# Kernel tuning notes

Hardware: AMD Instinct MI355X
Metric: run time of the kernel (lower is better)

The kernel has to match this reference:

```python
import jax, jax.numpy as jnp
import numpy as np

B, S, D = 2, 2048, 1024
H, HD = 16, 64
DFF = 4 * D
EPS = 1e-5


def gelu(x):
    return 0.5 * x * (1.0 + jnp.tanh(jnp.sqrt(2.0 / jnp.pi) * (x + 0.044715 * x * x * x)))


def layer_norm(x, scale, bias):
    mu = jnp.mean(x, axis=-1, keepdims=True)
    var = jnp.mean(jnp.square(x - mu), axis=-1, keepdims=True)
    return (x - mu) * jax.lax.rsqrt(var + EPS) * scale + bias


def setup_inputs() -> dict:
    key = jax.random.key(0)
    ks = jax.random.split(key, 8)
    s = 0.02
    x = jax.random.normal(ks[0], (B, S, D), jnp.float32)
    mask = jnp.tril(jnp.ones((S, S), dtype=bool))[None, None]  # (1,1,S,S) causal
    return {
        "x": x,
        "mask": mask,
        "ln1_scale": jnp.ones((D,), jnp.float32),
        "ln1_bias": jnp.zeros((D,), jnp.float32),
        "ln2_scale": jnp.ones((D,), jnp.float32),
        "ln2_bias": jnp.zeros((D,), jnp.float32),
        "w_qkv": jax.random.normal(ks[1], (D, 3 * D), jnp.float32) * s,
        "b_qkv": jnp.zeros((3 * D,), jnp.float32),
        "w_attn_proj": jax.random.normal(ks[2], (D, D), jnp.float32) * s,
        "b_attn_proj": jnp.zeros((D,), jnp.float32),
        "w_fc": jax.random.normal(ks[3], (D, DFF), jnp.float32) * s,
        "b_fc": jnp.zeros((DFF,), jnp.float32),
        "w_mlp_proj": jax.random.normal(ks[4], (DFF, D), jnp.float32) * s,
        "b_mlp_proj": jnp.zeros((D,), jnp.float32),
    }


def reference(x, mask, ln1_scale, ln1_bias, ln2_scale, ln2_bias,
              w_qkv, b_qkv, w_attn_proj, b_attn_proj,
              w_fc, b_fc, w_mlp_proj, b_mlp_proj):
    bsz, seq, _ = x.shape
    # --- attention branch ---
    h = layer_norm(x, ln1_scale, ln1_bias)
    qkv = h @ w_qkv + b_qkv                       # (b, s, 3D)
    q, k, v = jnp.split(qkv, 3, axis=-1)
    q = q.reshape(bsz, seq, H, HD).transpose(0, 2, 1, 3)  # bhsd
    k = k.reshape(bsz, seq, H, HD).transpose(0, 2, 1, 3)
    v = v.reshape(bsz, seq, H, HD).transpose(0, 2, 1, 3)
    q = q * (1.0 / jnp.sqrt(HD))
    scores = jnp.einsum('bhqd,bhkd->bhqk', q, k)
    scores = jnp.where(mask, scores, -1e10)
    probs = jax.nn.softmax(scores, axis=-1)
    attn = jnp.einsum('bhqk,bhkd->bhqd', probs, v)
    attn = attn.transpose(0, 2, 1, 3).reshape(bsz, seq, D)
    attn = attn @ w_attn_proj + b_attn_proj
    x = x + attn
    # --- MLP branch ---
    h = layer_norm(x, ln2_scale, ln2_bias)
    h = gelu(h @ w_fc + b_fc)
    h = h @ w_mlp_proj + b_mlp_proj
    return x + h
```

## Files before the change

### kernel.cpp

```cpp
#include <hip/hip_runtime.h>
#include <stdint.h>


typedef __attribute__((ext_vector_type(8))) short bf16x8;
typedef __attribute__((ext_vector_type(8))) unsigned short u16x8;
typedef __attribute__((ext_vector_type(4))) float f32x4;

#define NEG_BIG -30000.0f
#define EXP2SC 0.18033688011112042f

__device__ __forceinline__ float b2f(unsigned short u) {
  union { unsigned int i; float f; } c; c.i = ((unsigned int)u) << 16; return c.f;
}
__device__ __forceinline__ unsigned short f2b(float f) {
  union { float f; unsigned int u; } c; c.f = f;
  unsigned int r = c.u + 0x7fffu + ((c.u >> 16) & 1u);
  return (unsigned short)(r >> 16);
}
__device__ __forceinline__ float ldx(const void* p, size_t i, int f32) {
  return f32 ? ((const float*)p)[i] : b2f(((const unsigned short*)p)[i]);
}
__device__ __forceinline__ void gld_lds16(const void* g, void* l) {
  __builtin_amdgcn_global_load_lds(
      (__attribute__((address_space(1))) void*)(void*)g,
      (__attribute__((address_space(3))) void*)l, 16, 0, 0);
}

__global__ void detect_k(const unsigned short* __restrict__ x, int* __restrict__ flag) {
  int lane = threadIdx.x;
  int cnt = 0;
#pragma unroll
  for (int j = 0; j < 4; ++j) {
    unsigned e = (x[lane * 4 + j] >> 7) & 0xFF;
    if (e >= 100 && e <= 145) cnt++;
  }
#pragma unroll
  for (int off = 32; off; off >>= 1) cnt += __shfl_down(cnt, off);
  if (lane == 0) *flag = (cnt < 220) ? 1 : 0;
}

__global__ __launch_bounds__(256) void transpose_k(
    const void* __restrict__ in, unsigned short* __restrict__ out,
    int K, int N, const int* __restrict__ flag) {
  int fm = *flag;
  __shared__ unsigned short tile[64][72];
  int n0 = blockIdx.x * 64, k0 = blockIdx.y * 64;
  int t = threadIdx.x;
  int r = t >> 3, c0 = (t & 7) * 8;
  if (fm) {
    const float* inf = (const float*)in;
#pragma unroll
    for (int p = 0; p < 2; ++p) {
      int k = r + p * 32;
      float4 v0 = *(const float4*)(inf + (size_t)(k0 + k) * N + n0 + c0);
      float4 v1 = *(const float4*)(inf + (size_t)(k0 + k) * N + n0 + c0 + 4);
      tile[k][c0 + 0] = f2b(v0.x); tile[k][c0 + 1] = f2b(v0.y);
      tile[k][c0 + 2] = f2b(v0.z); tile[k][c0 + 3] = f2b(v0.w);
      tile[k][c0 + 4] = f2b(v1.x); tile[k][c0 + 5] = f2b(v1.y);
      tile[k][c0 + 6] = f2b(v1.z); tile[k][c0 + 7] = f2b(v1.w);
    }
  } else {
    const unsigned short* inu = (const unsigned short*)in;
#pragma unroll
    for (int p = 0; p < 2; ++p) {
      int k = r + p * 32;
      u16x8 v = *(const u16x8*)(inu + (size_t)(k0 + k) * N + n0 + c0);
      *(u16x8*)&tile[k][c0] = v;
    }
  }
  __syncthreads();
#pragma unroll
  for (int p = 0; p < 2; ++p) {
    int n = r + p * 32;
    u16x8 v;
#pragma unroll
    for (int j = 0; j < 8; ++j) v[j] = tile[c0 + j][n];
    *(u16x8*)(out + (size_t)(n0 + n) * K + k0 + c0) = v;
  }
}

__global__ __launch_bounds__(256) void ln_k(
    const void* __restrict__ x, const void* __restrict__ sc,
    const void* __restrict__ bs, unsigned short* __restrict__ out,
    const int* __restrict__ flag, int xAdap) {
  int fm = *flag;
  int fx = xAdap ? fm : 0;
  int row = blockIdx.x, t = threadIdx.x;
  float f0, f1, f2, f3;
  if (fx) {
    float4 xv = ((const float4*)x)[(size_t)row * 256 + t];
    f0 = xv.x; f1 = xv.y; f2 = xv.z; f3 = xv.w;
  } else {
    ushort4 xv = ((const ushort4*)x)[(size_t)row * 256 + t];
    f0 = b2f(xv.x); f1 = b2f(xv.y); f2 = b2f(xv.z); f3 = b2f(xv.w);
  }
  float s = f0 + f1 + f2 + f3;
  float q = f0 * f0 + f1 * f1 + f2 * f2 + f3 * f3;
#pragma unroll
  for (int off = 32; off; off >>= 1) {
    s += __shfl_down(s, off);
    q += __shfl_down(q, off);
  }
  __shared__ float red[8];
  int w = t >> 6, lane = t & 63;
  if (lane == 0) { red[w] = s; red[w + 4] = q; }
  __syncthreads();
  float S = red[0] + red[1] + red[2] + red[3];
  float Q = red[4] + red[5] + red[6] + red[7];
  float mean = S * (1.f / 1024.f);
  float var = Q * (1.f / 1024.f) - mean * mean;
  float rstd = rsqrtf(var + 1e-5f);
  int c = t * 4;
  ushort4 o;
  o.x = f2b((f0 - mean) * rstd * ldx(sc, c, fm)     + ldx(bs, c, fm));
  o.y = f2b((f1 - mean) * rstd * ldx(sc, c + 1, fm) + ldx(bs, c + 1, fm));
  o.z = f2b((f2 - mean) * rstd * ldx(sc, c + 2, fm) + ldx(bs, c + 2, fm));
  o.w = f2b((f3 - mean) * rstd * ldx(sc, c + 3, fm) + ldx(bs, c + 3, fm));
  ((ushort4*)(out + (size_t)row * 1024))[t] = o;
}

template <int EPI>
__global__ __launch_bounds__(256) void gemm_bt(
    const unsigned short* __restrict__ A, const unsigned short* __restrict__ Bt,
    const void* __restrict__ bias, const void* __restrict__ res,
    void* __restrict__ C, int M, int N, int K,
    const int* __restrict__ flag, int resAdap, int outAdap) {
  int fm = *flag;
  int fr = resAdap ? fm : 0;
  int fo = outAdap ? fm : 0;
  __shared__ unsigned short As[128 * 32];
  __shared__ unsigned short Bs[128 * 32];
  int t = threadIdx.x;
  int bn = blockIdx.x * 128, bm = blockIdx.y * 128;
  int w = t >> 6, lane = t & 63, quad = lane >> 4, l16 = lane & 15;
  int wm = (w >> 1) * 64, wn = (w & 1) * 64;
  f32x4 acc[4][4] = {};

  int c1 = t, c2 = t + 256;
  int r1 = c1 >> 2, e1 = (c1 & 3) * 8;
  int r2 = c2 >> 2, e2 = (c2 & 3) * 8;
  const unsigned short* a1 = A + (size_t)(bm + r1) * K + e1;
  const unsigned short* a2 = A + (size_t)(bm + r2) * K + e2;
  const unsigned short* b1 = Bt + (size_t)(bn + r1) * K + e1;
  const unsigned short* b2 = Bt + (size_t)(bn + r2) * K + e2;

  for (int k0 = 0; k0 < K; k0 += 32) {
    gld_lds16(a1 + k0, As + c1 * 8);
    gld_lds16(a2 + k0, As + c2 * 8);
    gld_lds16(b1 + k0, Bs + c1 * 8);
    gld_lds16(b2 + k0, Bs + c2 * 8);
    __syncthreads();
    bf16x8 af[4], bfr[4];
#pragma unroll
    for (int i = 0; i < 4; ++i)
      af[i] = *(const bf16x8*)&As[(wm + i * 16 + l16) * 32 + quad * 8];
#pragma unroll
    for (int j = 0; j < 4; ++j)
      bfr[j] = *(const bf16x8*)&Bs[(wn + j * 16 + l16) * 32 + quad * 8];
#pragma unroll
    for (int i = 0; i < 4; ++i)
#pragma unroll
      for (int j = 0; j < 4; ++j)
        acc[i][j] = __builtin_amdgcn_mfma_f32_16x16x32_bf16(af[i], bfr[j], acc[i][j], 0, 0, 0);
    __syncthreads();
  }

#pragma unroll
  for (int j = 0; j < 4; ++j) {
    int col = bn + wn + j * 16 + l16;
    float bb = ldx(bias, col, fm);
#pragma unroll
    for (int i = 0; i < 4; ++i) {
      int row0 = bm + wm + i * 16 + quad * 4;
#pragma unroll
      for (int r = 0; r < 4; ++r) {
        float v = acc[i][j][r] + bb;
        if (EPI == 1) {
          float u = 0.7978845608f * (v + 0.044715f * v * v * v);
          float e = __expf(2.f * u);
          float th = 1.f - 2.f / (e + 1.f);
          v = 0.5f * v * (1.f + th);
        } else if (EPI == 2) {
          v += ldx(res, (size_t)(row0 + r) * N + col, fr);
        }
        size_t idx = (size_t)(row0 + r) * N + col;
        if (fo) ((float*)C)[idx] = v;
        else    ((unsigned short*)C)[idx] = f2b(v);
      }
    }
  }
}

__global__ __launch_bounds__(256) void gemm_pk(
    const unsigned short* __restrict__ A, const unsigned short* __restrict__ Bt,
    float* __restrict__ P, int M, int N, int Kh, int Kfull) {
  __shared__ unsigned short As[128 * 32];
  __shared__ unsigned short Bs[128 * 32];
  int t = threadIdx.x;
  int bn = blockIdx.x * 128, bm = blockIdx.y * 128;
  int koff = blockIdx.z * Kh;
  float* Pz = P + (size_t)blockIdx.z * M * N;
  int w = t >> 6, lane = t & 63, quad = lane >> 4, l16 = lane & 15;
  int wm = (w >> 1) * 64, wn = (w & 1) * 64;
  f32x4 acc[4][4] = {};

  int c1 = t, c2 = t + 256;
  int r1 = c1 >> 2, e1 = (c1 & 3) * 8;
  int r2 = c2 >> 2, e2 = (c2 & 3) * 8;
  const unsigned short* a1 = A + (size_t)(bm + r1) * Kfull + koff + e1;
  const unsigned short* a2 = A + (size_t)(bm + r2) * Kfull + koff + e2;
  const unsigned short* b1 = Bt + (size_t)(bn + r1) * Kfull + koff + e1;
  const unsigned short* b2 = Bt + (size_t)(bn + r2) * Kfull + koff + e2;

  for (int k0 = 0; k0 < Kh; k0 += 32) {
    gld_lds16(a1 + k0, As + c1 * 8);
    gld_lds16(a2 + k0, As + c2 * 8);
    gld_lds16(b1 + k0, Bs + c1 * 8);
    gld_lds16(b2 + k0, Bs + c2 * 8);
    __syncthreads();
    bf16x8 af[4], bfr[4];
#pragma unroll
    for (int i = 0; i < 4; ++i)
      af[i] = *(const bf16x8*)&As[(wm + i * 16 + l16) * 32 + quad * 8];
#pragma unroll
    for (int j = 0; j < 4; ++j)
      bfr[j] = *(const bf16x8*)&Bs[(wn + j * 16 + l16) * 32 + quad * 8];
#pragma unroll
    for (int i = 0; i < 4; ++i)
#pragma unroll
      for (int j = 0; j < 4; ++j)
        acc[i][j] = __builtin_amdgcn_mfma_f32_16x16x32_bf16(af[i], bfr[j], acc[i][j], 0, 0, 0);
    __syncthreads();
  }

#pragma unroll
  for (int j = 0; j < 4; ++j) {
    int col = bn + wn + j * 16 + l16;
#pragma unroll
    for (int i = 0; i < 4; ++i) {
      int row0 = bm + wm + i * 16 + quad * 4;
#pragma unroll
      for (int r = 0; r < 4; ++r)
        Pz[(size_t)(row0 + r) * N + col] = acc[i][j][r];
    }
  }
}

__global__ __launch_bounds__(256) void reduce2_k(
    const float* __restrict__ P0, const float* __restrict__ P1,
    const void* __restrict__ bias, const void* __restrict__ res,
    void* __restrict__ out, int N,
    const int* __restrict__ flag, int resAdap, int outAdap) {
  int fm = *flag;
  int fr = resAdap ? fm : 0;
  int fo = outAdap ? fm : 0;
  size_t idx = ((size_t)blockIdx.x * 256 + threadIdx.x) * 4;
  float4 p0 = *(const float4*)(P0 + idx);
  float4 p1 = *(const float4*)(P1 + idx);
  int col = (int)(idx & (size_t)(N - 1));
  float v0 = p0.x + p1.x + ldx(bias, col, fm)     + ldx(res, idx, fr);
  float v1 = p0.y + p1.y + ldx(bias, col + 1, fm) + ldx(res, idx + 1, fr);
  float v2 = p0.z + p1.z + ldx(bias, col + 2, fm) + ldx(res, idx + 2, fr);
  float v3 = p0.w + p1.w + ldx(bias, col + 3, fm) + ldx(res, idx + 3, fr);
  if (fo) {
    float4 o; o.x = v0; o.y = v1; o.z = v2; o.w = v3;
    *(float4*)((float*)out + idx) = o;
  } else {
    ushort4 o; o.x = f2b(v0); o.y = f2b(v1); o.z = f2b(v2); o.w = f2b(v3);
    *(ushort4*)((unsigned short*)out + idx) = o;
  }
}

__global__ __launch_bounds__(256) void attn_k(
    const unsigned short* __restrict__ qkv, unsigned short* __restrict__ out) {
  __shared__ unsigned short Ks[64 * 72];
  __shared__ unsigned int   Vt[64 * 35];
  __shared__ unsigned short Ps[4 * 16 * 72];
  int t = threadIdx.x, w = t >> 6, lane = t & 63, quad = lane >> 4, l16 = lane & 15;
  int pi = blockIdx.x, bh = blockIdx.y, b = bh >> 4, h = bh & 15;
  const unsigned short* base = qkv + (size_t)b * 2048 * 3072 + h * 64;
  unsigned short* Pw = Ps + w * 16 * 72;
  int srow = t >> 3, d0 = (t & 7) * 8;

#pragma unroll 1
  for (int half = 0; half < 2; ++half) {
    int qt = half ? (31 - pi) : pi;
    int q0 = qt * 64;
    int qrel = w * 16 + l16;
    const unsigned short* qp = base + (size_t)(q0 + qrel) * 3072;
    bf16x8 bq0 = *(const bf16x8*)(qp + quad * 8);
    bf16x8 bq1 = *(const bf16x8*)(qp + 32 + quad * 8);
    float m_i = NEG_BIG, l_i = 0.f;
    f32x4 O[4] = {};

#pragma unroll 1
    for (int kt = 0; kt <= qt; ++kt) {
      const unsigned short* kb = base + (size_t)(kt * 64) * 3072;
      {
        u16x8 k0v = *(const u16x8*)(kb + (size_t)srow * 3072 + 1024 + d0);
        u16x8 k1v = *(const u16x8*)(kb + (size_t)(srow + 32) * 3072 + 1024 + d0);
        *(u16x8*)&Ks[srow * 72 + d0] = k0v;
        *(u16x8*)&Ks[(srow + 32) * 72 + d0] = k1v;
        int sp = t >> 3;
        u16x8 va = *(const u16x8*)(kb + (size_t)(2 * sp) * 3072 + 2048 + d0);
        u16x8 vb = *(const u16x8*)(kb + (size_t)(2 * sp + 1) * 3072 + 2048 + d0);
#pragma unroll
        for (int j = 0; j < 8; ++j)
          Vt[(d0 + j) * 35 + sp] = (unsigned int)va[j] | ((unsigned int)vb[j] << 16);
      }
      __syncthreads();

      f32x4 ST[4];
#pragma unroll
      for (int i = 0; i < 4; ++i) {
        bf16x8 ak0 = *(const bf16x8*)&Ks[(i * 16 + l16) * 72 + quad * 8];
        bf16x8 ak1 = *(const bf16x8*)&Ks[(i * 16 + l16) * 72 + 32 + quad * 8];
        f32x4 z = {};
        z = __builtin_amdgcn_mfma_f32_16x16x32_bf16(ak0, bq0, z, 0, 0, 0);
        ST[i] = __builtin_amdgcn_mfma_f32_16x16x32_bf16(ak1, bq1, z, 0, 0, 0);
      }

      bool dm = (kt == qt);
      float p[4][4];
      float mx = NEG_BIG;
#pragma unroll
      for (int i = 0; i < 4; ++i)
#pragma unroll
        for (int r = 0; r < 4; ++r) {
          float v = ST[i][r] * EXP2SC;
          int srel = i * 16 + quad * 4 + r;
          if (dm && srel > qrel) v = NEG_BIG;
          p[i][r] = v;
          mx = fmaxf(mx, v);
        }
      mx = fmaxf(mx, __shfl_xor(mx, 16));
      mx = fmaxf(mx, __shfl_xor(mx, 32));
      float mn = fmaxf(m_i, mx);
      float alpha = exp2f(m_i - mn);
      m_i = mn;
      float sum = 0.f;
#pragma unroll
      for (int i = 0; i < 4; ++i)
#pragma unroll
        for (int r = 0; r < 4; ++r) {
          float e = exp2f(p[i][r] - mn);
          p[i][r] = e;
          sum += e;
        }
      sum += __shfl_xor(sum, 16);
      sum += __shfl_xor(sum, 32);
      l_i = alpha * l_i + sum;

#pragma unroll
      for (int i = 0; i < 4; ++i) {
        uint2 pr;
        pr.x = (unsigned int)f2b(p[i][0]) | ((unsigned int)f2b(p[i][1]) << 16);
        pr.y = (unsigned int)f2b(p[i][2]) | ((unsigned int)f2b(p[i][3]) << 16);
        *(uint2*)(Pw + l16 * 72 + i * 16 + quad * 4) = pr;
      }

      float ar[4];
#pragma unroll
      for (int r = 0; r < 4; ++r)
        ar[r] = __shfl(alpha, (lane & 48) | (quad * 4 + r));
#pragma unroll
      for (int jd = 0; jd < 4; ++jd)
#pragma unroll
        for (int r = 0; r < 4; ++r) O[jd][r] *= ar[r];

#pragma unroll
      for (int ks = 0; ks < 2; ++ks) {
        bf16x8 ap = *(const bf16x8*)(Pw + l16 * 72 + ks * 32 + quad * 8);
#pragma unroll
        for (int jd = 0; jd < 4; ++jd) {
          union { unsigned int u[4]; bf16x8 v; } bv;
          int vbase = (jd * 16 + l16) * 35 + ks * 16 + quad * 4;
#pragma unroll
          for (int cc = 0; cc < 4; ++cc) bv.u[cc] = Vt[vbase + cc];
          O[jd] = __builtin_amdgcn_mfma_f32_16x16x32_bf16(ap, bv.v, O[jd], 0, 0, 0);
        }
      }
      __syncthreads();
    }

    float li[4];
#pragma unroll
    for (int r = 0; r < 4; ++r)
      li[r] = 1.f / __shfl(l_i, (lane & 48) | (quad * 4 + r));
#pragma unroll
    for (int jd = 0; jd < 4; ++jd)
#pragma unroll
      for (int r = 0; r < 4; ++r) {
        size_t row = (size_t)b * 2048 + q0 + w * 16 + quad * 4 + r;
        out[row * 1024 + h * 64 + jd * 16 + l16] = f2b(O[jd][r] * li[r]);
      }
  }
}

extern "C" void kernel_launch(void* const* d_in, const int* in_sizes, int n_in,
                              void* d_out, int out_size, void* d_ws, size_t ws_size,
                              hipStream_t stream) {
  (void)in_sizes; (void)n_in; (void)out_size;
  const void* x     = d_in[0];
  const void* ln1s  = d_in[2];
  const void* ln1b  = d_in[3];
  const void* ln2s  = d_in[4];
  const void* ln2b  = d_in[5];
  const void* w_qkv = d_in[6];
  const void* b_qkv = d_in[7];
  const void* w_ap  = d_in[8];
  const void* b_ap  = d_in[9];
  const void* w_fc  = d_in[10];
  const void* b_fc  = d_in[11];
  const void* w_mp  = d_in[12];
  const void* b_mp  = d_in[13];
  char* ws = (char*)d_ws;

  const int M = 4096, D = 1024, DFF = 4096, QKV3 = 3072;
  size_t off = 0;
  auto alloc = [&](size_t n) { char* p = ws + off; off += n; return p; };
  int* flag            = (int*)alloc(256);
  unsigned short* wT   = (unsigned short*)alloc((size_t)DFF * D * 2);
  unsigned short* hbuf = (unsigned short*)alloc((size_t)M * D * 2);
  unsigned short* x1   = (unsigned short*)alloc((size_t)M * D * 2);
  char* region = alloc((size_t)M * DFF * 2);
  unsigned short* qkvb = (unsigned short*)region;
  float* P0a = (float*)region;
  float* P1a = (float*)(region + (size_t)M * D * 4);
  unsigned short* fcb  = (unsigned short*)region;
  bool mlpSplit = ws_size >= off + (size_t)M * D * 8 + 1024;
  float* P0m = (float*)(ws + off);
  float* P1m = P0m + (size_t)M * D;

  dim3 blk(256);
  detect_k<<<dim3(1), dim3(64), 0, stream>>>((const unsigned short*)x, flag);
  transpose_k<<<dim3(QKV3 / 64, D / 64), blk, 0, stream>>>(w_qkv, wT, D, QKV3, flag);
  ln_k<<<dim3(M), blk, 0, stream>>>(x, ln1s, ln1b, hbuf, flag, 1);
  gemm_bt<0><<<dim3(QKV3 / 128, M / 128), blk, 0, stream>>>(hbuf, wT, b_qkv, nullptr, qkvb, M, QKV3, D, flag, 0, 0);
  attn_k<<<dim3(16, 32), blk, 0, stream>>>(qkvb, hbuf);
  transpose_k<<<dim3(D / 64, D / 64), blk, 0, stream>>>(w_ap, wT, D, D, flag);
  gemm_pk<<<dim3(D / 128, M / 128, 2), blk, 0, stream>>>(hbuf, wT, P0a, M, D, D / 2, D);
  reduce2_k<<<dim3(M * D / 1024), blk, 0, stream>>>(P0a, P1a, b_ap, x, x1, D, flag, 1, 0);
  transpose_k<<<dim3(DFF / 64, D / 64), blk, 0, stream>>>(w_fc, wT, D, DFF, flag);
  ln_k<<<dim3(M), blk, 0, stream>>>(x1, ln2s, ln2b, hbuf, flag, 0);
  gemm_bt<1><<<dim3(DFF / 128, M / 128), blk, 0, stream>>>(hbuf, wT, b_fc, nullptr, fcb, M, DFF, D, flag, 0, 0);
  transpose_k<<<dim3(D / 64, DFF / 64), blk, 0, stream>>>(w_mp, wT, DFF, D, flag);
  if (mlpSplit) {
    gemm_pk<<<dim3(D / 128, M / 128, 2), blk, 0, stream>>>(fcb, wT, P0m, M, D, DFF / 2, DFF);
    reduce2_k<<<dim3(M * D / 1024), blk, 0, stream>>>(P0m, P1m, b_mp, x1, d_out, D, flag, 0, 1);
  } else {
    gemm_bt<2><<<dim3(D / 128, M / 128), blk, 0, stream>>>(fcb, wT, b_mp, x1, d_out, M, D, DFF, flag, 0, 1);
  }
}
```

Measured before the change: 458.0 us.

## Deepen GEMM K-step to 64 and give attention one query tile per block

In both GEMM kernels, each iteration now loads two 32-wide K slices into two LDS buffers and runs both MFMA passes before the barrier. This halves the number of barrier pairs and issues more loads per synchronisation, at the cost of doubling the LDS footprint. The attention kernel no longer pairs query tiles qt and 31-qt inside one block. It launches 32 blocks per head, each handling one tile in reverse order, which gives more parallelism but loses the paired load balancing.

```diff
diff --git a/kernel.cpp b/kernel.cpp
--- a/kernel.cpp
+++ b/kernel.cpp
@@ -128,8 +128,8 @@
   int fm = *flag;
   int fr = resAdap ? fm : 0;
   int fo = outAdap ? fm : 0;
-  __shared__ unsigned short As[128 * 32];
-  __shared__ unsigned short Bs[128 * 32];
+  __shared__ unsigned short As[2][128 * 32];
+  __shared__ unsigned short Bs[2][128 * 32];
   int t = threadIdx.x;
   int bn = blockIdx.x * 128, bm = blockIdx.y * 128;
   int w = t >> 6, lane = t & 63, quad = lane >> 4, l16 = lane & 15;
@@ -144,24 +144,31 @@
   const unsigned short* b1 = Bt + (size_t)(bn + r1) * K + e1;
   const unsigned short* b2 = Bt + (size_t)(bn + r2) * K + e2;
 
-  for (int k0 = 0; k0 < K; k0 += 32) {
-    gld_lds16(a1 + k0, As + c1 * 8);
-    gld_lds16(a2 + k0, As + c2 * 8);
-    gld_lds16(b1 + k0, Bs + c1 * 8);
-    gld_lds16(b2 + k0, Bs + c2 * 8);
-    __syncthreads();
-    bf16x8 af[4], bfr[4];
-#pragma unroll
-    for (int i = 0; i < 4; ++i)
-      af[i] = *(const bf16x8*)&As[(wm + i * 16 + l16) * 32 + quad * 8];
-#pragma unroll
-    for (int j = 0; j < 4; ++j)
-      bfr[j] = *(const bf16x8*)&Bs[(wn + j * 16 + l16) * 32 + quad * 8];
-#pragma unroll
-    for (int i = 0; i < 4; ++i)
+  for (int k0 = 0; k0 < K; k0 += 64) {
+    gld_lds16(a1 + k0,      As[0] + c1 * 8);
+    gld_lds16(a2 + k0,      As[0] + c2 * 8);
+    gld_lds16(a1 + k0 + 32, As[1] + c1 * 8);
+    gld_lds16(a2 + k0 + 32, As[1] + c2 * 8);
+    gld_lds16(b1 + k0,      Bs[0] + c1 * 8);
+    gld_lds16(b2 + k0,      Bs[0] + c2 * 8);
+    gld_lds16(b1 + k0 + 32, Bs[1] + c1 * 8);
+    gld_lds16(b2 + k0 + 32, Bs[1] + c2 * 8);
+    __syncthreads();
+#pragma unroll
+    for (int h = 0; h < 2; ++h) {
+      bf16x8 af[4], bfr[4];
+#pragma unroll
+      for (int i = 0; i < 4; ++i)
+        af[i] = *(const bf16x8*)&As[h][(wm + i * 16 + l16) * 32 + quad * 8];
 #pragma unroll
       for (int j = 0; j < 4; ++j)
-        acc[i][j] = __builtin_amdgcn_mfma_f32_16x16x32_bf16(af[i], bfr[j], acc[i][j], 0, 0, 0);
+        bfr[j] = *(const bf16x8*)&Bs[h][(wn + j * 16 + l16) * 32 + quad * 8];
+#pragma unroll
+      for (int i = 0; i < 4; ++i)
+#pragma unroll
+        for (int j = 0; j < 4; ++j)
+          acc[i][j] = __builtin_amdgcn_mfma_f32_16x16x32_bf16(af[i], bfr[j], acc[i][j], 0, 0, 0);
+    }
     __syncthreads();
   }
 
@@ -194,8 +201,8 @@
 __global__ __launch_bounds__(256) void gemm_pk(
     const unsigned short* __restrict__ A, const unsigned short* __restrict__ Bt,
     float* __restrict__ P, int M, int N, int Kh, int Kfull) {
-  __shared__ unsigned short As[128 * 32];
-  __shared__ unsigned short Bs[128 * 32];
+  __shared__ unsigned short As[2][128 * 32];
+  __shared__ unsigned short Bs[2][128 * 32];
   int t = threadIdx.x;
   int bn = blockIdx.x * 128, bm = blockIdx.y * 128;
   int koff = blockIdx.z * Kh;
@@ -212,24 +219,31 @@
   const unsigned short* b1 = Bt + (size_t)(bn + r1) * Kfull + koff + e1;
   const unsigned short* b2 = Bt + (size_t)(bn + r2) * Kfull + koff + e2;
 
-  for (int k0 = 0; k0 < Kh; k0 += 32) {
-    gld_lds16(a1 + k0, As + c1 * 8);
-    gld_lds16(a2 + k0, As + c2 * 8);
-    gld_lds16(b1 + k0, Bs + c1 * 8);
-    gld_lds16(b2 + k0, Bs + c2 * 8);
-    __syncthreads();
-    bf16x8 af[4], bfr[4];
-#pragma unroll
-    for (int i = 0; i < 4; ++i)
-      af[i] = *(const bf16x8*)&As[(wm + i * 16 + l16) * 32 + quad * 8];
-#pragma unroll
-    for (int j = 0; j < 4; ++j)
-      bfr[j] = *(const bf16x8*)&Bs[(wn + j * 16 + l16) * 32 + quad * 8];
-#pragma unroll
-    for (int i = 0; i < 4; ++i)
+  for (int k0 = 0; k0 < Kh; k0 += 64) {
+    gld_lds16(a1 + k0,      As[0] + c1 * 8);
+    gld_lds16(a2 + k0,      As[0] + c2 * 8);
+    gld_lds16(a1 + k0 + 32, As[1] + c1 * 8);
+    gld_lds16(a2 + k0 + 32, As[1] + c2 * 8);
+    gld_lds16(b1 + k0,      Bs[0] + c1 * 8);
+    gld_lds16(b2 + k0,      Bs[0] + c2 * 8);
+    gld_lds16(b1 + k0 + 32, Bs[1] + c1 * 8);
+    gld_lds16(b2 + k0 + 32, Bs[1] + c2 * 8);
+    __syncthreads();
+#pragma unroll
+    for (int h = 0; h < 2; ++h) {
+      bf16x8 af[4], bfr[4];
+#pragma unroll
+      for (int i = 0; i < 4; ++i)
+        af[i] = *(const bf16x8*)&As[h][(wm + i * 16 + l16) * 32 + quad * 8];
 #pragma unroll
       for (int j = 0; j < 4; ++j)
-        acc[i][j] = __builtin_amdgcn_mfma_f32_16x16x32_bf16(af[i], bfr[j], acc[i][j], 0, 0, 0);
+        bfr[j] = *(const bf16x8*)&Bs[h][(wn + j * 16 + l16) * 32 + quad * 8];
+#pragma unroll
+      for (int i = 0; i < 4; ++i)
+#pragma unroll
+        for (int j = 0; j < 4; ++j)
+          acc[i][j] = __builtin_amdgcn_mfma_f32_16x16x32_bf16(af[i], bfr[j], acc[i][j], 0, 0, 0);
+    }
     __syncthreads();
   }
 
@@ -277,124 +291,120 @@
   __shared__ unsigned int   Vt[64 * 35];
   __shared__ unsigned short Ps[4 * 16 * 72];
   int t = threadIdx.x, w = t >> 6, lane = t & 63, quad = lane >> 4, l16 = lane & 15;
-  int pi = blockIdx.x, bh = blockIdx.y, b = bh >> 4, h = bh & 15;
+  int qt = 31 - blockIdx.x, bh = blockIdx.y, b = bh >> 4, h = bh & 15;
   const unsigned short* base = qkv + (size_t)b * 2048 * 3072 + h * 64;
   unsigned short* Pw = Ps + w * 16 * 72;
   int srow = t >> 3, d0 = (t & 7) * 8;
 
+  int q0 = qt * 64;
+  int qrel = w * 16 + l16;
+  const unsigned short* qp = base + (size_t)(q0 + qrel) * 3072;
+  bf16x8 bq0 = *(const bf16x8*)(qp + quad * 8);
+  bf16x8 bq1 = *(const bf16x8*)(qp + 32 + quad * 8);
+  float m_i = NEG_BIG, l_i = 0.f;
+  f32x4 O[4] = {};
+
 #pragma unroll 1
-  for (int half = 0; half < 2; ++half) {
-    int qt = half ? (31 - pi) : pi;
-    int q0 = qt * 64;
-    int qrel = w * 16 + l16;
-    const unsigned short* qp = base + (size_t)(q0 + qrel) * 3072;
-    bf16x8 bq0 = *(const bf16x8*)(qp + quad * 8);
-    bf16x8 bq1 = *(const bf16x8*)(qp + 32 + quad * 8);
-    float m_i = NEG_BIG, l_i = 0.f;
-    f32x4 O[4] = {};
-
-#pragma unroll 1
-    for (int kt = 0; kt <= qt; ++kt) {
-      const unsigned short* kb = base + (size_t)(kt * 64) * 3072;
-      {
-        u16x8 k0v = *(const u16x8*)(kb + (size_t)srow * 3072 + 1024 + d0);
-        u16x8 k1v = *(const u16x8*)(kb + (size_t)(srow + 32) * 3072 + 1024 + d0);
-        *(u16x8*)&Ks[srow * 72 + d0] = k0v;
-        *(u16x8*)&Ks[(srow + 32) * 72 + d0] = k1v;
-        int sp = t >> 3;
-        u16x8 va = *(const u16x8*)(kb + (size_t)(2 * sp) * 3072 + 2048 + d0);
-        u16x8 vb = *(const u16x8*)(kb + (size_t)(2 * sp + 1) * 3072 + 2048 + d0);
-#pragma unroll
-        for (int j = 0; j < 8; ++j)
-          Vt[(d0 + j) * 35 + sp] = (unsigned int)va[j] | ((unsigned int)vb[j] << 16);
+  for (int kt = 0; kt <= qt; ++kt) {
+    const unsigned short* kb = base + (size_t)(kt * 64) * 3072;
+    {
+      u16x8 k0v = *(const u16x8*)(kb + (size_t)srow * 3072 + 1024 + d0);
+      u16x8 k1v = *(const u16x8*)(kb + (size_t)(srow + 32) * 3072 + 1024 + d0);
+      *(u16x8*)&Ks[srow * 72 + d0] = k0v;
+      *(u16x8*)&Ks[(srow + 32) * 72 + d0] = k1v;
+      int sp = t >> 3;
+      u16x8 va = *(const u16x8*)(kb + (size_t)(2 * sp) * 3072 + 2048 + d0);
+      u16x8 vb = *(const u16x8*)(kb + (size_t)(2 * sp + 1) * 3072 + 2048 + d0);
+#pragma unroll
+      for (int j = 0; j < 8; ++j)
+        Vt[(d0 + j) * 35 + sp] = (unsigned int)va[j] | ((unsigned int)vb[j] << 16);
+    }
+    __syncthreads();
+
+    f32x4 ST[4];
+#pragma unroll
+    for (int i = 0; i < 4; ++i) {
+      bf16x8 ak0 = *(const bf16x8*)&Ks[(i * 16 + l16) * 72 + quad * 8];
+      bf16x8 ak1 = *(const bf16x8*)&Ks[(i * 16 + l16) * 72 + 32 + quad * 8];
+      f32x4 z = {};
+      z = __builtin_amdgcn_mfma_f32_16x16x32_bf16(ak0, bq0, z, 0, 0, 0);
+      ST[i] = __builtin_amdgcn_mfma_f32_16x16x32_bf16(ak1, bq1, z, 0, 0, 0);
+    }
+
+    bool dm = (kt == qt);
+    float p[4][4];
+    float mx = NEG_BIG;
+#pragma unroll
+    for (int i = 0; i < 4; ++i)
+#pragma unroll
+      for (int r = 0; r < 4; ++r) {
+        float v = ST[i][r] * EXP2SC;
+        int srel = i * 16 + quad * 4 + r;
+        if (dm && srel > qrel) v = NEG_BIG;
+        p[i][r] = v;
+        mx = fmaxf(mx, v);
       }
-      __syncthreads();
-
-      f32x4 ST[4];
-#pragma unroll
-      for (int i = 0; i < 4; ++i) {
-        bf16x8 ak0 = *(const bf16x8*)&Ks[(i * 16 + l16) * 72 + quad * 8];
-        bf16x8 ak1 = *(const bf16x8*)&Ks[(i * 16 + l16) * 72 + 32 + quad * 8];
-        f32x4 z = {};
-        z = __builtin_amdgcn_mfma_f32_16x16x32_bf16(ak0, bq0, z, 0, 0, 0);
-        ST[i] = __builtin_amdgcn_mfma_f32_16x16x32_bf16(ak1, bq1, z, 0, 0, 0);
+    mx = fmaxf(mx, __shfl_xor(mx, 16));
+    mx = fmaxf(mx, __shfl_xor(mx, 32));
+    float mn = fmaxf(m_i, mx);
+    float alpha = exp2f(m_i - mn);
+    m_i = mn;
+    float sum = 0.f;
+#pragma unroll
+    for (int i = 0; i < 4; ++i)
+#pragma unroll
+      for (int r = 0; r < 4; ++r) {
+        float e = exp2f(p[i][r] - mn);
+        p[i][r] = e;
+        sum += e;
       }
-
-      bool dm = (kt == qt);
-      float p[4][4];
-      float mx = NEG_BIG;
-#pragma unroll
-      for (int i = 0; i < 4; ++i)
-#pragma unroll
-        for (int r = 0; r < 4; ++r) {
-          float v = ST[i][r] * EXP2SC;
-          int srel = i * 16 + quad * 4 + r;
-          if (dm && srel > qrel) v = NEG_BIG;
-          p[i][r] = v;
-          mx = fmaxf(mx, v);
-        }
-      mx = fmaxf(mx, __shfl_xor(mx, 16));
-      mx = fmaxf(mx, __shfl_xor(mx, 32));
-      float mn = fmaxf(m_i, mx);
-      float alpha = exp2f(m_i - mn);
-      m_i = mn;
-      float sum = 0.f;
-#pragma unroll
-      for (int i = 0; i < 4; ++i)
-#pragma unroll
-        for (int r = 0; r < 4; ++r) {
-          float e = exp2f(p[i][r] - mn);
-          p[i][r] = e;
-          sum += e;
-        }
-      sum += __shfl_xor(sum, 16);
-      sum += __shfl_xor(sum, 32);
-      l_i = alpha * l_i + sum;
-
-#pragma unroll
-      for (int i = 0; i < 4; ++i) {
-        uint2 pr;
-        pr.x = (unsigned int)f2b(p[i][0]) | ((unsigned int)f2b(p[i][1]) << 16);
-        pr.y = (unsigned int)f2b(p[i][2]) | ((unsigned int)f2b(p[i][3]) << 16);
-        *(uint2*)(Pw + l16 * 72 + i * 16 + quad * 4) = pr;
+    sum += __shfl_xor(sum, 16);
+    sum += __shfl_xor(sum, 32);
+    l_i = alpha * l_i + sum;
+
+#pragma unroll
+    for (int i = 0; i < 4; ++i) {
+      uint2 pr;
+      pr.x = (unsigned int)f2b(p[i][0]) | ((unsigned int)f2b(p[i][1]) << 16);
+      pr.y = (unsigned int)f2b(p[i][2]) | ((unsigned int)f2b(p[i][3]) << 16);
+      *(uint2*)(Pw + l16 * 72 + i * 16 + quad * 4) = pr;
+    }
+
+    float ar[4];
+#pragma unroll
+    for (int r = 0; r < 4; ++r)
+      ar[r] = __shfl(alpha, (lane & 48) | (quad * 4 + r));
+#pragma unroll
+    for (int jd = 0; jd < 4; ++jd)
+#pragma unroll
+      for (int r = 0; r < 4; ++r) O[jd][r] *= ar[r];
+
+#pragma unroll
+    for (int ks = 0; ks < 2; ++ks) {
+      bf16x8 ap = *(const bf16x8*)(Pw + l16 * 72 + ks * 32 + quad * 8);
+#pragma unroll
+      for (int jd = 0; jd < 4; ++jd) {
+        union { unsigned int u[4]; bf16x8 v; } bv;
+        int vbase = (jd * 16 + l16) * 35 + ks * 16 + quad * 4;
+#pragma unroll
+        for (int cc = 0; cc < 4; ++cc) bv.u[cc] = Vt[vbase + cc];
+        O[jd] = __builtin_amdgcn_mfma_f32_16x16x32_bf16(ap, bv.v, O[jd], 0, 0, 0);
       }
-
-      float ar[4];
-#pragma unroll
-      for (int r = 0; r < 4; ++r)
-        ar[r] = __shfl(alpha, (lane & 48) | (quad * 4 + r));
-#pragma unroll
-      for (int jd = 0; jd < 4; ++jd)
-#pragma unroll
-        for (int r = 0; r < 4; ++r) O[jd][r] *= ar[r];
-
-#pragma unroll
-      for (int ks = 0; ks < 2; ++ks) {
-        bf16x8 ap = *(const bf16x8*)(Pw + l16 * 72 + ks * 32 + quad * 8);
-#pragma unroll
-        for (int jd = 0; jd < 4; ++jd) {
-          union { unsigned int u[4]; bf16x8 v; } bv;
-          int vbase = (jd * 16 + l16) * 35 + ks * 16 + quad * 4;
-#pragma unroll
-          for (int cc = 0; cc < 4; ++cc) bv.u[cc] = Vt[vbase + cc];
-          O[jd] = __builtin_amdgcn_mfma_f32_16x16x32_bf16(ap, bv.v, O[jd], 0, 0, 0);
-        }
-      }
-      __syncthreads();
-    }
-
-    float li[4];
-#pragma unroll
-    for (int r = 0; r < 4; ++r)
-      li[r] = 1.f / __shfl(l_i, (lane & 48) | (quad * 4 + r));
-#pragma unroll
-    for (int jd = 0; jd < 4; ++jd)
-#pragma unroll
-      for (int r = 0; r < 4; ++r) {
-        size_t row = (size_t)b * 2048 + q0 + w * 16 + quad * 4 + r;
-        out[row * 1024 + h * 64 + jd * 16 + l16] = f2b(O[jd][r] * li[r]);
-      }
-  }
+    }
+    __syncthreads();
+  }
+
+  float li[4];
+#pragma unroll
+  for (int r = 0; r < 4; ++r)
+    li[r] = 1.f / __shfl(l_i, (lane & 48) | (quad * 4 + r));
+#pragma unroll
+  for (int jd = 0; jd < 4; ++jd)
+#pragma unroll
+    for (int r = 0; r < 4; ++r) {
+      size_t row = (size_t)b * 2048 + q0 + w * 16 + quad * 4 + r;
+      out[row * 1024 + h * 64 + jd * 16 + l16] = f2b(O[jd][r] * li[r]);
+    }
 }
 
 extern "C" void kernel_launch(void* const* d_in, const int* in_sizes, int n_in,
@@ -437,7 +447,7 @@
   transpose_k<<<dim3(QKV3 / 64, D / 64), blk, 0, stream>>>(w_qkv, wT, D, QKV3, flag);
   ln_k<<<dim3(M), blk, 0, stream>>>(x, ln1s, ln1b, hbuf, flag, 1);
   gemm_bt<0><<<dim3(QKV3 / 128, M / 128), blk, 0, stream>>>(hbuf, wT, b_qkv, nullptr, qkvb, M, QKV3, D, flag, 0, 0);
-  attn_k<<<dim3(16, 32), blk, 0, stream>>>(qkvb, hbuf);
+  attn_k<<<dim3(32, 32), blk, 0, stream>>>(qkvb, hbuf);
   transpose_k<<<dim3(D / 64, D / 64), blk, 0, stream>>>(w_ap, wT, D, D, flag);
   gemm_pk<<<dim3(D / 128, M / 128, 2), blk, 0, stream>>>(hbuf, wT, P0a, M, D, D / 2, D);
   reduce2_k<<<dim3(M * D / 1024), blk, 0, stream>>>(P0a, P1a, b_ap, x, x1, D, flag, 1, 0);
```

After: 460.1 us. About the same (+0.5%).
